# Performance work log

Hardware: AMD Instinct MI355X
Metric: run time of the kernel (lower is better)

## Reference

```python
import jax, jax.numpy as jnp
import numpy as np


def _hamming(n):
    # torch.hamming_window(n, periodic=False): 0.54 - 0.46*cos(2*pi*i/(n-1))
    if n == 1:
        return jnp.ones((1,), jnp.float32)
    i = jnp.arange(n, dtype=jnp.float32)
    return 0.54 - 0.46 * jnp.cos(2.0 * jnp.pi * i / (n - 1))


def setup_inputs() -> dict:
    key = jax.random.key(0)
    k1, k2, k3 = jax.random.split(key, 3)
    N, CIN, COUT, K = 4, 16, 32, 3
    D, H, W = 16, 64, 64
    x = jax.random.normal(k1, (N, CIN, D, H, W), dtype=jnp.float32)
    # Conv3d default init: U(-1/sqrt(fan_in), 1/sqrt(fan_in)), fan_in = cin*k^3
    bound = 1.0 / np.sqrt(CIN * K * K * K)
    weight = jax.random.uniform(k2, (COUT, CIN, K, K, K), jnp.float32, -bound, bound)
    bias = jax.random.uniform(k3, (COUT,), jnp.float32, -bound, bound)
    gamma = jnp.ones((COUT,), jnp.float32)   # BatchNorm3d weight
    beta = jnp.zeros((COUT,), jnp.float32)   # BatchNorm3d bias
    return {"x": x, "weight": weight, "bias": bias, "gamma": gamma, "beta": beta}


def reference(x, weight, bias, gamma, beta):
    # --- shrink_conv_weights: per-(cout,cin) soft-threshold, fully vectorized ---
    cutoff = weight.max(axis=(2, 3, 4), keepdims=True) * 0.5          # [cout,cin,1,1,1]
    shrunk = jnp.sign(weight) * jax.nn.relu(jnp.abs(weight) - cutoff / 100.0)
    w = jnp.where(weight < cutoff, shrunk, weight)
    # --- hamming window over the 3 kernel dims ---
    kd, kh, kw = w.shape[2], w.shape[3], w.shape[4]
    win = _hamming(kd)[:, None, None] * _hamming(kh)[None, :, None] * _hamming(kw)[None, None, :]
    w = w * win[None, None]                                           # [cout,cin,kd,kh,kw]
    # --- conv3d, padding='same' ---
    y = jax.lax.conv_general_dilated(
        x, w, window_strides=(1, 1, 1), padding="SAME",
        dimension_numbers=("NCDHW", "OIDHW", "NCDHW"))
    y = y + bias[None, :, None, None, None]
    # --- BatchNorm3d (training mode: batch stats, biased variance, eps=1e-5) ---
    mean = y.mean(axis=(0, 2, 3, 4), keepdims=True)
    var = y.var(axis=(0, 2, 3, 4), keepdims=True)
    y = (y - mean) * jax.lax.rsqrt(var + 1e-5)
    y = y * gamma[None, :, None, None, None] + beta[None, :, None, None, None]
    # --- softplus nonlinearity ---
    return jax.nn.softplus(y)
```

## Files before the change

### kernel.cpp

```cpp
#include <hip/hip_runtime.h>
#include <math.h>

#define N_    4
#define CIN   16
#define COUT  32
#define DD    16
#define HH_   64
#define WW_   64
#define MCNT  262144.0f

typedef __attribute__((ext_vector_type(8))) short short8;
typedef __attribute__((ext_vector_type(4))) float floatx4;

__device__ __forceinline__ ushort f2bf(float f) {
    uint u = __float_as_uint(f);
    uint r = (u + 0x7fffu + ((u >> 16) & 1u)) >> 16;
    return (ushort)r;
}
__device__ __forceinline__ float bf2f(ushort v) {
    return __uint_as_float(((uint)v) << 16);
}
__device__ __forceinline__ float softplus_f(float z) {
    return fmaxf(z, 0.0f) + log1pf(expf(-fabsf(z)));
}

#define FAST_XT_F    0
#define FAST_WB_F    2162688
#define FAST_SC_F    2169856
#define FAST_PART_F  2169920
#define FAST_YB_F    2301056
#define FAST_BYTES_FP32Y  ((size_t)FAST_YB_F * 4)
#define FAST_BYTES_BF16Y  ((size_t)(FAST_YB_F + 4194304) * 4)
#define XROW_U16     1056
#define XROW_CHUNKS  132

__global__ void prep_w(const float* __restrict__ weight, ushort* __restrict__ wb) {
    int t = threadIdx.x;
    int cout = t >> 4, cin = t & 15;
    const float* wp = weight + (cout * CIN + cin) * 27;
    float wv[27];
    float mx = -INFINITY;
    #pragma unroll
    for (int k = 0; k < 27; ++k) { wv[k] = wp[k]; mx = fmaxf(mx, wv[k]); }
    float cutoff = mx * 0.5f;
    const float win[3] = {0.08f, 1.0f, 0.08f};
    #pragma unroll
    for (int k = 0; k < 27; ++k) {
        float w = wv[k];
        float sg = (w > 0.0f) ? 1.0f : ((w < 0.0f) ? -1.0f : 0.0f);
        float shr = sg * fmaxf(fabsf(w) - cutoff * 0.01f, 0.0f);
        float o = (w < cutoff) ? shr : w;
        int kd = k / 9, kr = k % 9, kh = kr / 3, kw = kr % 3;
        o *= win[kd] * win[kh] * win[kw];
        int q = (kd * 3 + kh) * 3 + kw;
        int grp = q >> 1, half = q & 1;
        wb[(grp * COUT + cout) * 32 + half * 16 + cin] = f2bf(o);
    }
    wb[(13 * COUT + cout) * 32 + 16 + cin] = 0;
}

__global__ __launch_bounds__(256, 4)
void conv256(const float* __restrict__ x, const ushort* __restrict__ wb,
             const float* __restrict__ bias, ushort* __restrict__ yb,
             float* __restrict__ part) {
    __shared__ ushort xs[12 * XROW_U16];
    __shared__ float sred[4][64];

    int b = blockIdx.x;
    int n = b >> 9, d = (b >> 5) & 15, h0 = (b & 31) * 2;
    int t = threadIdx.x;
    int l = t & 63;
    int wv_ = t >> 6;
    int hq = wv_ >> 1, cf = wv_ & 1;
    int h = h0 + hq;
    int s = l & 15, g = l >> 4;
    int ghi = g >> 1;

    ((float*)sred)[t] = 0.0f;

    short8 A[14];
    #pragma unroll
    for (int grp = 0; grp < 14; ++grp)
        A[grp] = *(const short8*)&wb[(grp * COUT + cf * 16 + s) * 32 + g * 8];

    if (t < 24) {
        int row = t >> 1, cq = t & 1;
        uint4 z = {0u, 0u, 0u, 0u};
        *(uint4*)&xs[row * XROW_U16 + 0 * 16 + cq * 8]  = z;
        *(uint4*)&xs[row * XROW_U16 + 65 * 16 + cq * 8] = z;
    }
    const int CSTRIDE = DD * HH_ * WW_;
    for (int i = t; i < 1536; i += 256) {
        int row = i >> 7;
        int rem = i & 127;
        int cq = rem >> 6;
        int w  = rem & 63;
        int zdi = row >> 2, rh = row & 3;
        int zd = d - 1 + zdi, zh = h0 - 1 + rh;
        uint4 pk = {0u, 0u, 0u, 0u};
        if ((unsigned)zd < DD && (unsigned)zh < HH_) {
            const float* p0 = x + (((size_t)(n * CIN + cq * 8) * DD + zd) * HH_ + zh) * WW_ + w;
            float v0 = p0[0 * CSTRIDE], v1 = p0[1 * CSTRIDE];
            float v2 = p0[2 * CSTRIDE], v3 = p0[3 * CSTRIDE];
            float v4 = p0[4 * CSTRIDE], v5 = p0[5 * CSTRIDE];
            float v6 = p0[6 * CSTRIDE], v7 = p0[7 * CSTRIDE];
            pk.x = (uint)f2bf(v0) | ((uint)f2bf(v1) << 16);
            pk.y = (uint)f2bf(v2) | ((uint)f2bf(v3) << 16);
            pk.z = (uint)f2bf(v4) | ((uint)f2bf(v5) << 16);
            pk.w = (uint)f2bf(v6) | ((uint)f2bf(v7) << 16);
        }
        *(uint4*)&xs[row * XROW_U16 + (w + 1) * 16 + cq * 8] = pk;
    }
    __syncthreads();

    floatx4 acc[4];
    #pragma unroll
    for (int wf = 0; wf < 4; ++wf) acc[wf] = (floatx4){0.f, 0.f, 0.f, 0.f};

    int hbase = hq * XROW_U16 + s * 16 + (g & 1) * 8;

    #pragma unroll
    for (int grp = 0; grp < 14; ++grp) {
        const int qa = 2 * grp;
        const int qb = (grp == 13) ? 26 : 2 * grp + 1;
        const int t9a = qa / 3, t9b = qb / 3;
        const int ca = ((t9a / 3) * 4 + (t9a % 3)) * XROW_U16 + (qa % 3) * 16;
        const int cb = ((t9b / 3) * 4 + (t9b % 3)) * XROW_U16 + (qb % 3) * 16;
        int baddr = hbase + (ghi ? cb : ca);
        #pragma unroll
        for (int wf = 0; wf < 4; ++wf) {
            short8 B = *(const short8*)&xs[baddr + wf * 256];
            acc[wf] = __builtin_amdgcn_mfma_f32_16x16x32_bf16(A[grp], B, acc[wf], 0, 0, 0);
        }
    }

    float s1[4], s2[4];
    #pragma unroll
    for (int j = 0; j < 4; ++j) { s1[j] = 0.f; s2[j] = 0.f; }
    #pragma unroll
    for (int j = 0; j < 4; ++j) {
        int co = cf * 16 + g * 4 + j;
        float bval = bias[co];
        size_t obase = ((size_t)(n * COUT + co) * DD + d) * (HH_ * WW_) + h * WW_ + s;
        #pragma unroll
        for (int wf = 0; wf < 4; ++wf) {
            float val = acc[wf][j] + bval;
            yb[obase + wf * 16] = f2bf(val);
            s1[j] += val;
            s2[j] += val * val;
        }
    }
    #pragma unroll
    for (int m = 1; m < 16; m <<= 1) {
        #pragma unroll
        for (int j = 0; j < 4; ++j) {
            s1[j] += __shfl_xor(s1[j], m);
            s2[j] += __shfl_xor(s2[j], m);
        }
    }
    if (s == 0) {
        #pragma unroll
        for (int j = 0; j < 4; ++j) {
            int co = cf * 16 + g * 4 + j;
            sred[wv_][co]      = s1[j];
            sred[wv_][32 + co] = s2[j];
        }
    }
    __syncthreads();
    if (t < 64) {
        int cfh = (t >> 4) & 1;
        float v = sred[cfh][t] + sred[2 + cfh][t];
        part[(size_t)b * 64 + t] = v;
    }
}

template <int NBLK>
__global__ __launch_bounds__(1024)
void stats_fast_t(const float* __restrict__ part, const float* __restrict__ gamma,
                  const float* __restrict__ beta, float* __restrict__ scale,
                  float* __restrict__ shift) {
    __shared__ float red[16][64];
    __shared__ float tot[64];
    const int RPG = NBLK / 16;
    int t = threadIdx.x;
    int c = t & 63, rg = t >> 6;
    const float* p = part + (size_t)rg * RPG * 64 + c;
    float s = 0.f;
    #pragma unroll 8
    for (int r = 0; r < RPG; ++r) s += p[r * 64];
    red[rg][c] = s;
    __syncthreads();
    if (t < 64) {
        float v = 0.f;
        #pragma unroll
        for (int r = 0; r < 16; ++r) v += red[r][t];
        tot[t] = v;
    }
    __syncthreads();
    if (t < 32) {
        float mean = tot[t] / MCNT;
        float var  = tot[32 + t] / MCNT - mean * mean;
        float rstd = rsqrtf(var + 1e-5f);
        float sc = gamma[t] * rstd;
        scale[t] = sc;
        shift[t] = beta[t] - mean * sc;
    }
}

__global__ __launch_bounds__(256)
void bn_act_bf16(const ushort* __restrict__ yb, float* __restrict__ out,
                 const float* __restrict__ scale, const float* __restrict__ shift) {
    const int NV8 = (N_ * COUT * DD * HH_ * WW_) / 8;
    int stride = gridDim.x * blockDim.x;
    const short8* y8 = (const short8*)yb;
    for (int i = blockIdx.x * blockDim.x + threadIdx.x; i < NV8; i += stride) {
        int ch = (i >> 13) & 31;
        float sc = scale[ch];
        float sh = shift[ch];
        short8 yv = y8[i];
        float4 o0, o1;
        float* op0 = (float*)&o0;
        float* op1 = (float*)&o1;
        #pragma unroll
        for (int j = 0; j < 4; ++j) {
            float z = bf2f((ushort)yv[j]) * sc + sh;
            op0[j] = softplus_f(z);
        }
        #pragma unroll
        for (int j = 0; j < 4; ++j) {
            float z = bf2f((ushort)yv[4 + j]) * sc + sh;
            op1[j] = softplus_f(z);
        }
        *(float4*)&out[(size_t)i * 8]     = o0;
        *(float4*)&out[(size_t)i * 8 + 4] = o1;
    }
}

__global__ __launch_bounds__(256, 4)
void transpose_prep(const float* __restrict__ x, const float* __restrict__ weight,
                    ushort* __restrict__ xt, ushort* __restrict__ wb) {
    __shared__ ushort lds[4 * 64 * 16];
    int b = blockIdx.x;
    int n = b >> 8, d = (b >> 4) & 15, h0 = (b & 15) * 4;
    int t = threadIdx.x;

    if (b == 0) {
        #pragma unroll
        for (int rep = 0; rep < 2; ++rep) {
            int p = t + rep * 256;
            int cout = p >> 4, cin = p & 15;
            const float* wp = weight + (cout * CIN + cin) * 27;
            float wv[27];
            float mx = -INFINITY;
            #pragma unroll
            for (int k = 0; k < 27; ++k) { wv[k] = wp[k]; mx = fmaxf(mx, wv[k]); }
            float cutoff = mx * 0.5f;
            const float win[3] = {0.08f, 1.0f, 0.08f};
            #pragma unroll
            for (int k = 0; k < 27; ++k) {
                float w = wv[k];
                float sg = (w > 0.0f) ? 1.0f : ((w < 0.0f) ? -1.0f : 0.0f);
                float shr = sg * fmaxf(fabsf(w) - cutoff * 0.01f, 0.0f);
                float o = (w < cutoff) ? shr : w;
                int kd = k / 9, kr = k % 9, kh = kr / 3, kw = kr % 3;
                o *= win[kd] * win[kh] * win[kw];
                int q = (kd * 3 + kh) * 3 + kw;
                int grp = q >> 1, half = q & 1;
                wb[(grp * COUT + cout) * 32 + half * 16 + cin] = f2bf(o);
            }
            wb[(13 * COUT + cout) * 32 + 16 + cin] = 0;
        }
    }

    int hh = t >> 6, w = t & 63;
    const float* xp = x + ((size_t)(n * CIN * DD + d) * HH_ + (h0 + hh)) * WW_ + w;
    const int CSTRIDE = DD * HH_ * WW_;
    uint rowv[8];
    #pragma unroll
    for (int cp = 0; cp < 8; ++cp) {
        float a  = xp[(2 * cp)     * CSTRIDE];
        float b2 = xp[(2 * cp + 1) * CSTRIDE];
        rowv[cp] = (uint)f2bf(a) | ((uint)f2bf(b2) << 16);
    }
    #pragma unroll
    for (int cp = 0; cp < 8; ++cp)
        *(uint*)&lds[(hh * 64 + w) * 16 + 2 * cp] = rowv[cp];
    __syncthreads();
    uint* xtg = (uint*)xt;
    for (int i = t; i < 4 * 528; i += 256) {
        int hh2 = i / 528, u = i - hh2 * 528;
        int slot = u >> 3, cp = u & 7;
        uint val = 0;
        if (slot >= 1 && slot <= 64)
            val = *(uint*)&lds[(hh2 * 64 + (slot - 1)) * 16 + 2 * cp];
        xtg[(size_t)((n * DD + d) * HH_ + (h0 + hh2)) * 528 + u] = val;
    }
}

__global__ __launch_bounds__(512, 4)
void conv_mfma_f32y(const ushort* __restrict__ xt, const ushort* __restrict__ wb,
                    const float* __restrict__ bias, float* __restrict__ outf,
                    float* __restrict__ part) {
    __shared__ ushort xs[18 * XROW_U16];
    __shared__ float sred[8][64];

    int b = blockIdx.x;
    int n = b >> 8, d = (b >> 4) & 15, h0 = (b & 15) * 4;
    int t = threadIdx.x;
    int l = t & 63;
    int wv_ = t >> 6;
    int hq = wv_ >> 1, cf = wv_ & 1;
    int h = h0 + hq;
    int s = l & 15, g = l >> 4;
    int ghi = g >> 1;

    ((float*)sred)[t] = 0.0f;

    short8 A[14];
    #pragma unroll
    for (int grp = 0; grp < 14; ++grp)
        A[grp] = *(const short8*)&wb[(grp * COUT + cf * 16 + s) * 32 + g * 8];

    const uint4* xt4 = (const uint4*)xt;
    uint4* xs4 = (uint4*)xs;
    for (int i = t; i < 18 * XROW_CHUNKS; i += 512) {
        int row = i / XROW_CHUNKS, c = i - row * XROW_CHUNKS;
        int zdi = row / 6, rh = row - zdi * 6;
        int zd = d - 1 + zdi, zh = h0 - 1 + rh;
        uint4 v = {0u, 0u, 0u, 0u};
        if ((unsigned)zd < DD && (unsigned)zh < HH_)
            v = xt4[(size_t)((n * DD + zd) * HH_ + zh) * XROW_CHUNKS + c];
        xs4[i] = v;
    }
    __syncthreads();

    floatx4 acc[4];
    #pragma unroll
    for (int wf = 0; wf < 4; ++wf) acc[wf] = (floatx4){0.f, 0.f, 0.f, 0.f};

    int hbase = hq * XROW_U16 + s * 16 + (g & 1) * 8;

    #pragma unroll
    for (int grp = 0; grp < 14; ++grp) {
        const int qa = 2 * grp;
        const int qb = (grp == 13) ? 26 : 2 * grp + 1;
        const int t9a = qa / 3, t9b = qb / 3;
        const int ca = ((t9a / 3) * 6 + (t9a % 3)) * XROW_U16 + (qa % 3) * 16;
        const int cb = ((t9b / 3) * 6 + (t9b % 3)) * XROW_U16 + (qb % 3) * 16;
        int baddr = hbase + (ghi ? cb : ca);
        #pragma unroll
        for (int wf = 0; wf < 4; ++wf) {
            short8 B = *(const short8*)&xs[baddr + wf * 256];
            acc[wf] = __builtin_amdgcn_mfma_f32_16x16x32_bf16(A[grp], B, acc[wf], 0, 0, 0);
        }
    }

    float s1[4], s2[4];
    #pragma unroll
    for (int j = 0; j < 4; ++j) { s1[j] = 0.f; s2[j] = 0.f; }
    #pragma unroll
    for (int j = 0; j < 4; ++j) {
        int co = cf * 16 + g * 4 + j;
        float bval = bias[co];
        size_t obase = ((size_t)(n * COUT + co) * DD + d) * (HH_ * WW_) + h * WW_ + s;
        #pragma unroll
        for (int wf = 0; wf < 4; ++wf) {
            float val = acc[wf][j] + bval;
            outf[obase + wf * 16] = val;
            s1[j] += val;
            s2[j] += val * val;
        }
    }
    #pragma unroll
    for (int m = 1; m < 16; m <<= 1) {
        #pragma unroll
        for (int j = 0; j < 4; ++j) {
            s1[j] += __shfl_xor(s1[j], m);
            s2[j] += __shfl_xor(s2[j], m);
        }
    }
    if (s == 0) {
        #pragma unroll
        for (int j = 0; j < 4; ++j) {
            int co = cf * 16 + g * 4 + j;
            sred[wv_][co]      = s1[j];
            sred[wv_][32 + co] = s2[j];
        }
    }
    __syncthreads();
    if (t < 64) {
        int cfh = (t >> 4) & 1;
        float v = sred[cfh][t] + sred[2 + cfh][t] + sred[4 + cfh][t] + sred[6 + cfh][t];
        part[(size_t)b * 64 + t] = v;
    }
}

__global__ void bn_act_kernel(float* __restrict__ out, const float* __restrict__ scale,
                              const float* __restrict__ shift) {
    const int NV4 = (N_ * COUT * DD * HH_ * WW_) / 4;
    int stride = gridDim.x * blockDim.x;
    float4* o4 = (float4*)out;
    for (int i = blockIdx.x * blockDim.x + threadIdx.x; i < NV4; i += stride) {
        int ch = (i >> 14) & 31;
        float sc = scale[ch];
        float sh = shift[ch];
        float4 val = o4[i];
        float* vp = (float*)&val;
        #pragma unroll
        for (int j = 0; j < 4; ++j) {
            float z = vp[j] * sc + sh;
            vp[j] = softplus_f(z);
        }
        o4[i] = val;
    }
}

#define WS_W      0
#define WS_SUM    13824
#define WS_SUMSQ  13856
#define WS_SCALE  13888
#define WS_SHIFT  13920

__global__ void prep_weights(const float* __restrict__ weight, float* __restrict__ ws) {
    int t = threadIdx.x;
    if (t < 64) ws[WS_SUM + t] = 0.0f;
    int cout = t >> 4, cin = t & 15;
    const float* wp = weight + (cout * CIN + cin) * 27;
    float wv[27];
    float mx = -INFINITY;
    #pragma unroll
    for (int k = 0; k < 27; ++k) { wv[k] = wp[k]; mx = fmaxf(mx, wv[k]); }
    float cutoff = mx * 0.5f;
    const float win[3] = {0.08f, 1.0f, 0.08f};
    #pragma unroll
    for (int k = 0; k < 27; ++k) {
        float w = wv[k];
        float s = (w > 0.0f) ? 1.0f : ((w < 0.0f) ? -1.0f : 0.0f);
        float shr = s * fmaxf(fabsf(w) - cutoff * 0.01f, 0.0f);
        float o = (w < cutoff) ? shr : w;
        int kd = k / 9, kr = k % 9, kh = kr / 3, kw = kr % 3;
        o *= win[kd] * win[kh] * win[kw];
        ws[WS_W + (cin * 27 + k) * COUT + cout] = o;
    }
}

#define RS 68
__global__ __launch_bounds__(256, 4)
void conv_kernel(const float* __restrict__ x, const float* __restrict__ bias,
                 const float* __restrict__ wsw, float* __restrict__ out,
                 float* __restrict__ sums, float* __restrict__ sumsqs) {
    __shared__ float xsf[3 * 6 * RS];
    __shared__ float sredf[16][8];
    int b = blockIdx.x;
    int n  = b >> 8;
    int d  = (b >> 4) & 15;
    int h0 = (b & 15) << 2;
    int tid = threadIdx.x;
    int wg = tid & 15;
    int cg2 = (tid >> 4) & 3;
    int v  = tid >> 6;
    int cohalf = v & 1;
    int hhalf  = v >> 1;
    int w0 = wg * 4;
    int co0 = cohalf * 16 + cg2 * 4;
    float acc[4][2][4];
    #pragma unroll
    for (int c = 0; c < 4; ++c)
        #pragma unroll
        for (int i = 0; i < 2; ++i)
            #pragma unroll
            for (int j = 0; j < 4; ++j) acc[c][i][j] = 0.0f;
    const float* xn = x + (size_t)n * CIN * DD * HH_ * WW_;
    for (int cin = 0; cin < CIN; ++cin) {
        __syncthreads();
        const float* xc = xn + cin * DD * HH_ * WW_;
        for (int idx = tid; idx < 3 * 6 * RS; idx += 256) {
            int row = idx / RS;
            int c   = idx - row * RS;
            int dd  = row / 6;
            int r   = row - dd * 6;
            int zd = d - 1 + dd;
            int zh = h0 - 1 + r;
            int w  = c - 1;
            float val = 0.0f;
            if ((unsigned)zd < DD && (unsigned)zh < HH_ && (unsigned)w < WW_)
                val = xc[(zd * HH_ + zh) * WW_ + w];
            xsf[idx] = val;
        }
        __syncthreads();
        const float* wc = wsw + cin * 27 * COUT + co0;
        #pragma unroll 1
        for (int kd = 0; kd < 3; ++kd) {
            float4 wvv[9];
            #pragma unroll
            for (int j = 0; j < 9; ++j)
                wvv[j] = *(const float4*)&wc[(kd * 9 + j) * COUT];
            const float* xp = &xsf[(kd * 6 + hhalf * 2) * RS];
            #pragma unroll
            for (int rr = 0; rr < 4; ++rr) {
                const float* xr_ = &xp[rr * RS + w0];
                float4 xm = *(const float4*)xr_;
                float x4 = xr_[4];
                float x5 = xr_[5];
                float xv[6] = {xm.x, xm.y, xm.z, xm.w, x4, x5};
                #pragma unroll
                for (int kh = 0; kh < 3; ++kh) {
                    int i = rr - kh;
                    if (i < 0 || i > 1) continue;
                    #pragma unroll
                    for (int kw = 0; kw < 3; ++kw) {
                        float4 w4 = wvv[kh * 3 + kw];
                        #pragma unroll
                        for (int j = 0; j < 4; ++j) {
                            float xx = xv[j + kw];
                            acc[0][i][j] = fmaf(w4.x, xx, acc[0][i][j]);
                            acc[1][i][j] = fmaf(w4.y, xx, acc[1][i][j]);
                            acc[2][i][j] = fmaf(w4.z, xx, acc[2][i][j]);
                            acc[3][i][j] = fmaf(w4.w, xx, acc[3][i][j]);
                        }
                    }
                }
            }
        }
    }
    float s1[4], s2[4];
    #pragma unroll
    for (int c = 0; c < 4; ++c) {
        float bval = bias[co0 + c];
        s1[c] = 0.0f; s2[c] = 0.0f;
        #pragma unroll
        for (int i = 0; i < 2; ++i) {
            float4 o;
            float* op = (float*)&o;
            #pragma unroll
            for (int j = 0; j < 4; ++j) {
                float val = acc[c][i][j] + bval;
                op[j] = val;
                s1[c] += val;
                s2[c] += val * val;
            }
            int hh = h0 + hhalf * 2 + i;
            *(float4*)&out[((((size_t)n * COUT + co0 + c) * DD + d) * HH_ + hh) * WW_ + w0] = o;
        }
    }
    #pragma unroll
    for (int m = 1; m < 16; m <<= 1) {
        #pragma unroll
        for (int c = 0; c < 4; ++c) {
            s1[c] += __shfl_xor(s1[c], m);
            s2[c] += __shfl_xor(s2[c], m);
        }
    }
    if ((tid & 15) == 0) {
        int gg = tid >> 4;
        #pragma unroll
        for (int c = 0; c < 4; ++c) { sredf[gg][c] = s1[c]; sredf[gg][4 + c] = s2[c]; }
    }
    __syncthreads();
    if (tid < 64) {
        int co   = tid & 31;
        int kind = tid >> 5;
        int ch   = (co >> 4) & 1;
        int cgg  = (co >> 2) & 3;
        int c    = co & 3;
        float val = sredf[ch * 4 + cgg][kind * 4 + c] + sredf[(ch + 2) * 4 + cgg][kind * 4 + c];
        atomicAdd(kind ? &sumsqs[co] : &sums[co], val);
    }
}

__global__ void stats_kernel(const float* __restrict__ gamma, const float* __restrict__ beta,
                             const float* __restrict__ sums, const float* __restrict__ sumsqs,
                             float* __restrict__ scale, float* __restrict__ shift) {
    int c = threadIdx.x;
    if (c >= 32) return;
    float mean = sums[c] / MCNT;
    float var  = sumsqs[c] / MCNT - mean * mean;
    float rstd = rsqrtf(var + 1e-5f);
    float sc = gamma[c] * rstd;
    scale[c] = sc;
    shift[c] = beta[c] - mean * sc;
}

extern "C" void kernel_launch(void* const* d_in, const int* in_sizes, int n_in,
                              void* d_out, int out_size, void* d_ws, size_t ws_size,
                              hipStream_t stream) {
    const float* x      = (const float*)d_in[0];
    const float* weight = (const float*)d_in[1];
    const float* bias   = (const float*)d_in[2];
    const float* gamma  = (const float*)d_in[3];
    const float* beta   = (const float*)d_in[4];
    float* out = (float*)d_out;
    float* wsf = (float*)d_ws;

    float* scale = wsf + FAST_SC_F;
    float* shift = wsf + FAST_SC_F + 32;
    float* part  = wsf + FAST_PART_F;
    ushort* wb   = (ushort*)(wsf + FAST_WB_F);

    if (ws_size >= FAST_BYTES_BF16Y) {
        ushort* yb = (ushort*)(wsf + FAST_YB_F);
        hipLaunchKernelGGL(prep_w, dim3(1), dim3(512), 0, stream, weight, wb);
        hipLaunchKernelGGL(conv256, dim3(2048), dim3(256), 0, stream,
                           x, wb, bias, yb, part);
        hipLaunchKernelGGL((stats_fast_t<2048>), dim3(1), dim3(1024), 0, stream,
                           part, gamma, beta, scale, shift);
        hipLaunchKernelGGL(bn_act_bf16, dim3(2048), dim3(256), 0, stream,
                           yb, out, scale, shift);
    } else if (ws_size >= FAST_BYTES_FP32Y) {
        ushort* xt = (ushort*)(wsf + FAST_XT_F);
        hipLaunchKernelGGL(transpose_prep, dim3(1024), dim3(256), 0, stream,
                           x, weight, xt, wb);
        hipLaunchKernelGGL(conv_mfma_f32y, dim3(1024), dim3(512), 0, stream,
                           xt, wb, bias, out, part);
        hipLaunchKernelGGL((stats_fast_t<1024>), dim3(1), dim3(1024), 0, stream,
                           part, gamma, beta, scale, shift);
        hipLaunchKernelGGL(bn_act_kernel, dim3(2048), dim3(256), 0, stream,
                           out, scale, shift);
    } else {
        hipLaunchKernelGGL(prep_weights, dim3(1), dim3(512), 0, stream, weight, wsf);
        hipLaunchKernelGGL(conv_kernel, dim3(1024), dim3(256), 0, stream,
                           x, bias, wsf + WS_W, out, wsf + WS_SUM, wsf + WS_SUMSQ);
        hipLaunchKernelGGL(stats_kernel, dim3(1), dim3(64), 0, stream,
                           gamma, beta, wsf + WS_SUM, wsf + WS_SUMSQ, wsf + WS_SCALE, wsf + WS_SHIFT);
        hipLaunchKernelGGL(bn_act_kernel, dim3(2048), dim3(256), 0, stream,
                           out, wsf + WS_SCALE, wsf + WS_SHIFT);
    }
}
```

Baseline: 62.18 us.

## Tile four output rows per block and loop both cout halves per wave

The conv kernel now handles four h rows per block instead of two. Each wave owns one row and loops over both 16-channel output halves, so the staged input halo is 6 rows per depth slice rather than 4. This lowers the redundant global reads and bf16 conversion of halo rows and halves the block count and partial-stat rows. The cost is more shared memory per block, weight fragments reloaded twice per wave, and longer serial work per wave with fewer blocks to hide latency.

Measured after the change: 59.09 us. -5.0%, faster.

```diff
diff --git a/kernel.cpp b/kernel.cpp
--- a/kernel.cpp
+++ b/kernel.cpp
@@ -60,42 +60,34 @@
 }
 
 __global__ __launch_bounds__(256, 4)
-void conv256(const float* __restrict__ x, const ushort* __restrict__ wb,
-             const float* __restrict__ bias, ushort* __restrict__ yb,
-             float* __restrict__ part) {
-    __shared__ ushort xs[12 * XROW_U16];
+void conv4w(const float* __restrict__ x, const ushort* __restrict__ wb,
+            const float* __restrict__ bias, ushort* __restrict__ yb,
+            float* __restrict__ part) {
+    __shared__ ushort xs[18 * XROW_U16];
     __shared__ float sred[4][64];
 
     int b = blockIdx.x;
-    int n = b >> 9, d = (b >> 5) & 15, h0 = (b & 31) * 2;
+    int n = b >> 8, d = (b >> 4) & 15, h0 = (b & 15) * 4;
     int t = threadIdx.x;
     int l = t & 63;
-    int wv_ = t >> 6;
-    int hq = wv_ >> 1, cf = wv_ & 1;
+    int hq = t >> 6;
     int h = h0 + hq;
     int s = l & 15, g = l >> 4;
     int ghi = g >> 1;
 
-    ((float*)sred)[t] = 0.0f;
-
-    short8 A[14];
-    #pragma unroll
-    for (int grp = 0; grp < 14; ++grp)
-        A[grp] = *(const short8*)&wb[(grp * COUT + cf * 16 + s) * 32 + g * 8];
-
-    if (t < 24) {
+    if (t < 36) {
         int row = t >> 1, cq = t & 1;
         uint4 z = {0u, 0u, 0u, 0u};
         *(uint4*)&xs[row * XROW_U16 + 0 * 16 + cq * 8]  = z;
         *(uint4*)&xs[row * XROW_U16 + 65 * 16 + cq * 8] = z;
     }
     const int CSTRIDE = DD * HH_ * WW_;
-    for (int i = t; i < 1536; i += 256) {
+    for (int i = t; i < 2304; i += 256) {
         int row = i >> 7;
         int rem = i & 127;
         int cq = rem >> 6;
         int w  = rem & 63;
-        int zdi = row >> 2, rh = row & 3;
+        int zdi = row / 6, rh = row - zdi * 6;
         int zd = d - 1 + zdi, zh = h0 - 1 + rh;
         uint4 pk = {0u, 0u, 0u, 0u};
         if ((unsigned)zd < DD && (unsigned)zh < HH_) {
@@ -113,63 +105,77 @@
     }
     __syncthreads();
 
-    floatx4 acc[4];
-    #pragma unroll
-    for (int wf = 0; wf < 4; ++wf) acc[wf] = (floatx4){0.f, 0.f, 0.f, 0.f};
-
     int hbase = hq * XROW_U16 + s * 16 + (g & 1) * 8;
-
-    #pragma unroll
-    for (int grp = 0; grp < 14; ++grp) {
-        const int qa = 2 * grp;
-        const int qb = (grp == 13) ? 26 : 2 * grp + 1;
-        const int t9a = qa / 3, t9b = qb / 3;
-        const int ca = ((t9a / 3) * 4 + (t9a % 3)) * XROW_U16 + (qa % 3) * 16;
-        const int cb = ((t9b / 3) * 4 + (t9b % 3)) * XROW_U16 + (qb % 3) * 16;
-        int baddr = hbase + (ghi ? cb : ca);
-        #pragma unroll
-        for (int wf = 0; wf < 4; ++wf) {
-            short8 B = *(const short8*)&xs[baddr + wf * 256];
-            acc[wf] = __builtin_amdgcn_mfma_f32_16x16x32_bf16(A[grp], B, acc[wf], 0, 0, 0);
-        }
-    }
-
-    float s1[4], s2[4];
-    #pragma unroll
-    for (int j = 0; j < 4; ++j) { s1[j] = 0.f; s2[j] = 0.f; }
-    #pragma unroll
-    for (int j = 0; j < 4; ++j) {
-        int co = cf * 16 + g * 4 + j;
-        float bval = bias[co];
-        size_t obase = ((size_t)(n * COUT + co) * DD + d) * (HH_ * WW_) + h * WW_ + s;
-        #pragma unroll
-        for (int wf = 0; wf < 4; ++wf) {
-            float val = acc[wf][j] + bval;
-            yb[obase + wf * 16] = f2bf(val);
-            s1[j] += val;
-            s2[j] += val * val;
-        }
-    }
-    #pragma unroll
-    for (int m = 1; m < 16; m <<= 1) {
-        #pragma unroll
-        for (int j = 0; j < 4; ++j) {
-            s1[j] += __shfl_xor(s1[j], m);
-            s2[j] += __shfl_xor(s2[j], m);
-        }
-    }
-    if (s == 0) {
+    float s1[2][4], s2[2][4];
+    #pragma unroll
+    for (int cf = 0; cf < 2; ++cf)
+        #pragma unroll
+        for (int j = 0; j < 4; ++j) { s1[cf][j] = 0.f; s2[cf][j] = 0.f; }
+
+    #pragma unroll
+    for (int cf = 0; cf < 2; ++cf) {
+        short8 A[14];
+        #pragma unroll
+        for (int grp = 0; grp < 14; ++grp)
+            A[grp] = *(const short8*)&wb[(grp * COUT + cf * 16 + s) * 32 + g * 8];
+
+        floatx4 acc[4];
+        #pragma unroll
+        for (int wf = 0; wf < 4; ++wf) acc[wf] = (floatx4){0.f, 0.f, 0.f, 0.f};
+
+        #pragma unroll
+        for (int grp = 0; grp < 14; ++grp) {
+            const int qa = 2 * grp;
+            const int qb = (grp == 13) ? 26 : 2 * grp + 1;
+            const int t9a = qa / 3, t9b = qb / 3;
+            const int ca = ((t9a / 3) * 6 + (t9a % 3)) * XROW_U16 + (qa % 3) * 16;
+            const int cb = ((t9b / 3) * 6 + (t9b % 3)) * XROW_U16 + (qb % 3) * 16;
+            int baddr = hbase + (ghi ? cb : ca);
+            #pragma unroll
+            for (int wf = 0; wf < 4; ++wf) {
+                short8 B = *(const short8*)&xs[baddr + wf * 256];
+                acc[wf] = __builtin_amdgcn_mfma_f32_16x16x32_bf16(A[grp], B, acc[wf], 0, 0, 0);
+            }
+        }
+
         #pragma unroll
         for (int j = 0; j < 4; ++j) {
             int co = cf * 16 + g * 4 + j;
-            sred[wv_][co]      = s1[j];
-            sred[wv_][32 + co] = s2[j];
-        }
+            float bval = bias[co];
+            size_t obase = ((size_t)(n * COUT + co) * DD + d) * (HH_ * WW_) + h * WW_ + s;
+            #pragma unroll
+            for (int wf = 0; wf < 4; ++wf) {
+                float val = acc[wf][j] + bval;
+                yb[obase + wf * 16] = f2bf(val);
+                s1[cf][j] += val;
+                s2[cf][j] += val * val;
+            }
+        }
+    }
+
+    #pragma unroll
+    for (int m = 1; m < 16; m <<= 1) {
+        #pragma unroll
+        for (int cf = 0; cf < 2; ++cf)
+            #pragma unroll
+            for (int j = 0; j < 4; ++j) {
+                s1[cf][j] += __shfl_xor(s1[cf][j], m);
+                s2[cf][j] += __shfl_xor(s2[cf][j], m);
+            }
+    }
+    if (s == 0) {
+        #pragma unroll
+        for (int cf = 0; cf < 2; ++cf)
+            #pragma unroll
+            for (int j = 0; j < 4; ++j) {
+                int co = cf * 16 + g * 4 + j;
+                sred[hq][co]      = s1[cf][j];
+                sred[hq][32 + co] = s2[cf][j];
+            }
     }
     __syncthreads();
     if (t < 64) {
-        int cfh = (t >> 4) & 1;
-        float v = sred[cfh][t] + sred[2 + cfh][t];
+        float v = sred[0][t] + sred[1][t] + sred[2][t] + sred[3][t];
         part[(size_t)b * 64 + t] = v;
     }
 }
@@ -600,9 +606,9 @@
     if (ws_size >= FAST_BYTES_BF16Y) {
         ushort* yb = (ushort*)(wsf + FAST_YB_F);
         hipLaunchKernelGGL(prep_w, dim3(1), dim3(512), 0, stream, weight, wb);
-        hipLaunchKernelGGL(conv256, dim3(2048), dim3(256), 0, stream,
+        hipLaunchKernelGGL(conv4w, dim3(1024), dim3(256), 0, stream,
                            x, wb, bias, yb, part);
-        hipLaunchKernelGGL((stats_fast_t<2048>), dim3(1), dim3(1024), 0, stream,
+        hipLaunchKernelGGL((stats_fast_t<1024>), dim3(1), dim3(1024), 0, stream,
                            part, gamma, beta, scale, shift);
         hipLaunchKernelGGL(bn_act_bf16, dim3(2048), dim3(256), 0, stream,
                            yb, out, scale, shift);
```
